# Optimization experiments

Hardware: AMD Instinct MI355X
Metric: run time of the kernel (lower is better)

The kernel has to match this reference:

```python
import jax, jax.numpy as jnp
import numpy as np

B, T, O = 32, 2048, 18            # batch, triples per graph, hardcoded object count
DIN1, H, DOUT = 1500, 512, 512    # net1 input dim is hardcoded 1500 in the source

def _kaiming(key, fan_in, fan_out):
    return jax.random.normal(key, (fan_in, fan_out), jnp.float32) * np.sqrt(2.0 / fan_in)

def setup_inputs() -> dict:
    key = jax.random.key(0)
    ks = jax.random.split(key, 8)
    trip = jax.random.normal(ks[0], (B, T, DIN1), jnp.float32)
    index = jax.random.randint(ks[1], (B, T, 2), 0, O)
    rel_lens = jax.random.randint(ks[2], (B,), 0, T)
    # net1: 1500 -> H -> 2H+Dout (ReLU after every layer incl. last)
    w1a = _kaiming(ks[3], DIN1, H); b1a = jnp.zeros((H,), jnp.float32)
    w1b = _kaiming(ks[4], H, 2 * H + DOUT); b1b = jnp.zeros((2 * H + DOUT,), jnp.float32)
    # net2: H -> H -> Dout (ReLU after every layer incl. last)
    w2a = _kaiming(ks[5], H, H); b2a = jnp.zeros((H,), jnp.float32)
    w2b = _kaiming(ks[6], H, DOUT); b2b = jnp.zeros((DOUT,), jnp.float32)
    return dict(trip=trip, index=index, rel_lens=rel_lens,
                w1a=w1a, b1a=b1a, w1b=w1b, b1b=b1b,
                w2a=w2a, b2a=b2a, w2b=w2b, b2b=b2b)

def reference(trip, index, rel_lens, w1a, b1a, w1b, b1b, w2a, b2a, w2b, b2b):
    # net1 MLP over all triples: [B,T,1500] -> [B,T,2H+Dout]
    h = jax.nn.relu(trip @ w1a + b1a)
    new_t = jax.nn.relu(h @ w1b + b1b)
    s_vecs = new_t[..., :H]              # [B,T,H] subject
    p_vecs = new_t[..., H:H + DOUT]      # [B,T,Dout] predicate (returned as-is)
    o_vecs = new_t[..., H + DOUT:]       # [B,T,H] object
    # mask out triples beyond rel_lens[i]
    mask = (jnp.arange(T)[None, :] < rel_lens[:, None]).astype(new_t.dtype)  # [B,T]
    oh_s = jax.nn.one_hot(index[..., 0], O, dtype=new_t.dtype) * mask[..., None]  # [B,T,O]
    oh_o = jax.nn.one_hot(index[..., 1], O, dtype=new_t.dtype) * mask[..., None]
    # per-batch scatter_add pooling into the O=18 object slots
    contrib = (jnp.einsum('bto,bth->boh', oh_s, s_vecs)
               + jnp.einsum('bto,bth->boh', oh_o, o_vecs))  # [B,O,H]
    # original code never resets pooled_obj_vecs inside the batch loop ->
    # accumulation is CUMULATIVE over batch items
    pooled = jnp.cumsum(contrib, axis=0)  # [B,O,H]
    # net2 MLP on each cumulative pool
    h2 = jax.nn.relu(pooled @ w2a + b2a)
    new_obj = jax.nn.relu(h2 @ w2b + b2b)  # [B,O,Dout]
    return new_obj, p_vecs
```

## Files before the change

### kernel.cpp

```cpp
#include <hip/hip_runtime.h>
#include <hip/hip_bf16.h>

#define NBATCH 32
#define NTIME  2048
#define NOBJ   18
#define KIN    1500
#define NH     512
#define NTOT   1536
#define NM     65536

typedef __attribute__((ext_vector_type(4))) float f32x4;
typedef __attribute__((ext_vector_type(8))) short s16x8;
typedef __attribute__((ext_vector_type(4))) short s16x4;

static __device__ __forceinline__ short f2bf(float f) {
  union { float f; unsigned u; } v; v.f = f;
  unsigned r = v.u + 0x7fffu + ((v.u >> 16) & 1u);
  return (short)(r >> 16);
}

static __device__ __forceinline__ void gload_lds16(const short* g, short* l) {
  __builtin_amdgcn_global_load_lds(
      (const __attribute__((address_space(1))) unsigned int*)(g),
      (__attribute__((address_space(3))) unsigned int*)(l), 16, 0, 0);
}

__global__ void k_prep(const float* __restrict__ src, short* __restrict__ dst,
                       int K, int Nsrc, int nkt, int total) {
  int i = blockIdx.x * 256 + threadIdx.x;
  if (i >= total) return;
  int chunk = i >> 14, off = i & 16383;
  int row = off >> 6, kcp = off & 63;
  int kc = kcp ^ ((row & 7) << 3);
  int cb = chunk / nkt, kt = chunk - cb * nkt;
  int n = cb * 256 + row, k = kt * 64 + kc;
  dst[i] = (k < K) ? f2bf(src[(size_t)k * Nsrc + n]) : (short)0;
}

__launch_bounds__(512, 2)
__global__ void k_gemm1(const float* __restrict__ A, const short* __restrict__ Bc,
                        const float* __restrict__ bias, short* __restrict__ Hc) {
  __shared__ short lA[2][64 * 64];
  __shared__ short lB[2][256 * 64];
  const int g = blockIdx.x;
  const int lid = (g & 7) * 256 + (g >> 3);
  const int rb = lid >> 1, cb = lid & 1;
  const int m0 = rb * 64, n0 = cb * 256;
  const int tid = threadIdx.x;
  const int lane = tid & 63, w = tid >> 6;
  const int wr = w >> 2, wc = w & 3;
  const int rlane = lane & 15, ksel = (lane >> 4) * 8;
  const int arow = tid >> 4;
  const int akq  = (tid & 15) * 4;
  const short* bchunk = Bc + (size_t)(cb * 24) * 16384;

  f32x4 acc[2][4] = {};
  float4 av[2];

  auto issue_stage = [&](int nb, int kt) {
    const int kbase = kt * 64;
    const bool fullq = (kt < 23) | (akq <= 24);
#pragma unroll
    for (int ri = 0; ri < 2; ++ri) {
      const float* p = A + (size_t)(m0 + arow + ri * 32) * KIN + kbase + akq;
      av[ri] = fullq ? *(const float4*)p : make_float4(0.f, 0.f, 0.f, 0.f);
    }
    const short* src = bchunk + (size_t)kt * 16384 + tid * 8;
#pragma unroll
    for (int i = 0; i < 4; ++i)
      gload_lds16(src + i * 4096, &lB[nb][tid * 8 + i * 4096]);
  };
  auto write_stage = [&](int nb) {
#pragma unroll
    for (int ri = 0; ri < 2; ++ri) {
      int row = arow + ri * 32;
      s16x4 h4;
      h4[0] = f2bf(av[ri].x); h4[1] = f2bf(av[ri].y);
      h4[2] = f2bf(av[ri].z); h4[3] = f2bf(av[ri].w);
      *(s16x4*)&lA[nb][row * 64 + (akq ^ ((row & 7) << 3))] = h4;
    }
  };
  auto compute = [&](int cu) {
#pragma unroll
    for (int j = 0; j < 2; ++j) {
      int k0 = j * 32 + ksel;
      s16x8 af[2], bfr[4];
#pragma unroll
      for (int m = 0; m < 2; ++m) {
        int row = wr * 32 + m * 16 + rlane;
        af[m] = *(const s16x8*)&lA[cu][row * 64 + (k0 ^ ((row & 7) << 3))];
      }
#pragma unroll
      for (int n = 0; n < 4; ++n) {
        int row = wc * 64 + n * 16 + rlane;
        bfr[n] = *(const s16x8*)&lB[cu][row * 64 + (k0 ^ ((row & 7) << 3))];
      }
#pragma unroll
      for (int m = 0; m < 2; ++m)
#pragma unroll
        for (int n = 0; n < 4; ++n)
          acc[m][n] = __builtin_amdgcn_mfma_f32_16x16x32_bf16(af[m], bfr[n], acc[m][n], 0, 0, 0);
    }
  };

  issue_stage(0, 0);
  write_stage(0);
  asm volatile("s_waitcnt vmcnt(0)" ::: "memory");
  __syncthreads();
  for (int kt = 0; kt < 24; ++kt) {
    const int cu = kt & 1;
    if (kt < 23) issue_stage(cu ^ 1, kt + 1);
    compute(cu);
    if (kt < 23) {
      write_stage(cu ^ 1);
      asm volatile("s_waitcnt vmcnt(0)" ::: "memory");
      __syncthreads();
    }
  }

#pragma unroll
  for (int n = 0; n < 4; ++n) {
    int c = n0 + wc * 64 + n * 16 + rlane;
    float bv = bias[c];
#pragma unroll
    for (int m = 0; m < 2; ++m) {
      int rbase = m0 + wr * 32 + m * 16 + ((lane >> 4) << 2);
#pragma unroll
      for (int q = 0; q < 4; ++q) {
        int r = rbase + q;
        float v = acc[m][n][q] + bv;
        v = v > 0.f ? v : 0.f;
        Hc[(size_t)(((r >> 7) * 8 + (c >> 6)) * 8192) + (r & 127) * 64 +
           ((c & 63) ^ ((r & 7) << 3))] = f2bf(v);
      }
    }
  }
}

__launch_bounds__(512, 2)
__global__ void k_gemm2(const short* __restrict__ Ac, const short* __restrict__ Bc,
                        const float* __restrict__ bias, const int* __restrict__ index,
                        const int* __restrict__ rel_lens,
                        float* __restrict__ contrib, float* __restrict__ out) {
  __shared__ short lA[2][64 * 64];
  __shared__ short lB[2][256 * 64];
  const int g = blockIdx.x;
  const int lid = (g & 7) * 768 + (g >> 3);
  const int rb = lid / 6, cb = lid - rb * 6;
  const int m0 = rb * 64, n0 = cb * 256;
  const int tid = threadIdx.x;
  const int lane = tid & 63, w = tid >> 6;
  const int wr = w >> 2, wc = w & 3;
  const int rlane = lane & 15, ksel = (lane >> 4) * 8;
  const short* achunk = Ac + (size_t)((m0 >> 7) * 8) * 8192 + (m0 & 127) * 64;
  const short* bchunk = Bc + (size_t)(cb * 8) * 16384;

  f32x4 acc[2][4] = {};

  auto issue_stage = [&](int nb, int kt) {
    gload_lds16(achunk + (size_t)kt * 8192 + tid * 8, &lA[nb][tid * 8]);
    const short* src = bchunk + (size_t)kt * 16384 + tid * 8;
#pragma unroll
    for (int i = 0; i < 4; ++i)
      gload_lds16(src + i * 4096, &lB[nb][tid * 8 + i * 4096]);
  };
  auto compute = [&](int cu) {
#pragma unroll
    for (int j = 0; j < 2; ++j) {
      int k0 = j * 32 + ksel;
      s16x8 af[2], bfr[4];
#pragma unroll
      for (int m = 0; m < 2; ++m) {
        int row = wr * 32 + m * 16 + rlane;
        af[m] = *(const s16x8*)&lA[cu][row * 64 + (k0 ^ ((row & 7) << 3))];
      }
#pragma unroll
      for (int n = 0; n < 4; ++n) {
        int row = wc * 64 + n * 16 + rlane;
        bfr[n] = *(const s16x8*)&lB[cu][row * 64 + (k0 ^ ((row & 7) << 3))];
      }
#pragma unroll
      for (int m = 0; m < 2; ++m)
#pragma unroll
        for (int n = 0; n < 4; ++n)
          acc[m][n] = __builtin_amdgcn_mfma_f32_16x16x32_bf16(af[m], bfr[n], acc[m][n], 0, 0, 0);
    }
  };

  issue_stage(0, 0);
  asm volatile("s_waitcnt vmcnt(0)" ::: "memory");
  __syncthreads();
  for (int kt = 0; kt < 8; ++kt) {
    const int cu = kt & 1;
    if (kt < 7) issue_stage(cu ^ 1, kt + 1);
    compute(cu);
    if (kt < 7) {
      asm volatile("s_waitcnt vmcnt(0)" ::: "memory");
      __syncthreads();
    }
  }

  const int region = n0 >> 9;
  float bv[4]; int cg[4];
#pragma unroll
  for (int n = 0; n < 4; ++n) { cg[n] = n0 + wc * 64 + n * 16 + rlane; bv[n] = bias[cg[n]]; }

  if (region == 1) {
    float* po = out + (size_t)NBATCH * NOBJ * NH;
#pragma unroll
    for (int m = 0; m < 2; ++m) {
      int rbase = m0 + wr * 32 + m * 16 + ((lane >> 4) << 2);
#pragma unroll
      for (int q = 0; q < 4; ++q) {
#pragma unroll
        for (int n = 0; n < 4; ++n) {
          float v = acc[m][n][q] + bv[n];
          v = v > 0.f ? v : 0.f;
          po[(size_t)(rbase + q) * NH + (cg[n] & 511)] = v;
        }
      }
    }
  } else {
    const int sel = region >> 1;
    const int b = m0 >> 11;
    const int rel = rel_lens[b];
#pragma unroll
    for (int m = 0; m < 2; ++m) {
      int rbase = m0 + wr * 32 + m * 16 + ((lane >> 4) << 2);
#pragma unroll
      for (int q = 0; q < 4; ++q) {
        int r = rbase + q;
        if ((r & 2047) < rel) {
          int idx = index[2 * r + sel];
          float* dst = contrib + ((b * NOBJ + idx) << 9);
#pragma unroll
          for (int n = 0; n < 4; ++n) {
            float v = acc[m][n][q] + bv[n];
            v = v > 0.f ? v : 0.f;
            atomicAdd(dst + (cg[n] & 511), v);
          }
        }
      }
    }
  }
}

__global__ void k_cumsum(const float* __restrict__ contrib, float* __restrict__ pooled) {
  int i = blockIdx.x * 256 + threadIdx.x;
  if (i >= NOBJ * NH) return;
  float a = 0.f;
#pragma unroll
  for (int b = 0; b < NBATCH; ++b) {
    a += contrib[b * (NOBJ * NH) + i];
    pooled[b * (NOBJ * NH) + i] = a;
  }
}

__global__ void k_mlp2(const float* __restrict__ pooled,
                       const float* __restrict__ w2a, const float* __restrict__ b2a,
                       const float* __restrict__ w2b, const float* __restrict__ b2b,
                       float* __restrict__ out) {
  __shared__ float pr[NH];
  __shared__ float hr[NH];
  int row = blockIdx.x;
  int tid = threadIdx.x;
  pr[tid]       = pooled[(size_t)row * NH + tid];
  pr[tid + 256] = pooled[(size_t)row * NH + tid + 256];
  __syncthreads();
  float s0 = 0.f, s1 = 0.f;
  for (int k = 0; k < NH; ++k) {
    float p = pr[k];
    s0 += p * w2a[k * NH + tid];
    s1 += p * w2a[k * NH + tid + 256];
  }
  s0 += b2a[tid]; s1 += b2a[tid + 256];
  hr[tid]       = s0 > 0.f ? s0 : 0.f;
  hr[tid + 256] = s1 > 0.f ? s1 : 0.f;
  __syncthreads();
  s0 = 0.f; s1 = 0.f;
  for (int k = 0; k < NH; ++k) {
    float h = hr[k];
    s0 += h * w2b[k * NH + tid];
    s1 += h * w2b[k * NH + tid + 256];
  }
  s0 += b2b[tid]; s1 += b2b[tid + 256];
  out[(size_t)row * NH + tid]       = s0 > 0.f ? s0 : 0.f;
  out[(size_t)row * NH + tid + 256] = s1 > 0.f ? s1 : 0.f;
}

extern "C" void kernel_launch(void* const* d_in, const int* in_sizes, int n_in,
                              void* d_out, int out_size, void* d_ws, size_t ws_size,
                              hipStream_t stream) {
  const float* trip     = (const float*)d_in[0];
  const int*   index    = (const int*)d_in[1];
  const int*   rel_lens = (const int*)d_in[2];
  const float* w1a      = (const float*)d_in[3];
  const float* b1a      = (const float*)d_in[4];
  const float* w1b      = (const float*)d_in[5];
  const float* b1b      = (const float*)d_in[6];
  const float* w2a      = (const float*)d_in[7];
  const float* b2a      = (const float*)d_in[8];
  const float* w2b      = (const float*)d_in[9];
  const float* b2b      = (const float*)d_in[10];
  float* out = (float*)d_out;

  char* ws = (char*)d_ws;
  short* wt1a    = (short*)(ws);
  short* wt1b    = (short*)(ws + 1572864);
  short* hbuf    = (short*)(ws + 3145728);
  float* contrib = (float*)(ws + 70254592);
  float* pooled  = contrib + NBATCH * NOBJ * NH;

  k_prep<<<3072, 256, 0, stream>>>(w1a, wt1a, KIN, NH, 24, NH * 1536);
  k_prep<<<3072, 256, 0, stream>>>(w1b, wt1b, NH, NTOT, 8, NTOT * NH);
  hipMemsetAsync(contrib, 0, (size_t)NBATCH * NOBJ * NH * sizeof(float), stream);
  k_gemm1<<<2048, 512, 0, stream>>>(trip, wt1a, b1a, hbuf);
  k_gemm2<<<6144, 512, 0, stream>>>(hbuf, wt1b, b1b, index, rel_lens, contrib, out);
  k_cumsum<<<36, 256, 0, stream>>>(contrib, pooled);
  k_mlp2<<<576, 256, 0, stream>>>(pooled, w2a, b2a, w2b, b2b, out);
}
```

Before: 480.4 us.

## Enlarge GEMM tiles to 256x256 with quadrant-interleaved loads and MFMA

Both GEMM kernels move from 64x256 to 256x256 output tiles, giving each wave 8x4 accumulators so every LDS fragment feeds more MFMAs. The K-loop is split into four quadrant phases that interleave half-tile global-to-LDS loads with MFMA work, using partial vmcnt waits, raw barriers and s_setprio around the MFMA bursts. The layout of the intermediate H buffer changes to 256-row chunks to match. The goal is higher arithmetic intensity and less global and LDS traffic per FLOP. The cost is fewer blocks (512 and 1536), much higher register pressure, larger LDS use and fragile hand-tuned wait counts.

```diff
diff --git a/kernel.cpp b/kernel.cpp
--- a/kernel.cpp
+++ b/kernel.cpp
@@ -40,97 +40,133 @@
 __launch_bounds__(512, 2)
 __global__ void k_gemm1(const float* __restrict__ A, const short* __restrict__ Bc,
                         const float* __restrict__ bias, short* __restrict__ Hc) {
-  __shared__ short lA[2][64 * 64];
+  __shared__ short lA[2][256 * 64];
   __shared__ short lB[2][256 * 64];
   const int g = blockIdx.x;
-  const int lid = (g & 7) * 256 + (g >> 3);
+  const int lid = (g & 7) * 64 + (g >> 3);
   const int rb = lid >> 1, cb = lid & 1;
-  const int m0 = rb * 64, n0 = cb * 256;
+  const int m0 = rb * 256, n0 = cb * 256;
   const int tid = threadIdx.x;
   const int lane = tid & 63, w = tid >> 6;
   const int wr = w >> 2, wc = w & 3;
   const int rlane = lane & 15, ksel = (lane >> 4) * 8;
+  const int swz = (rlane & 7) << 3;
+  const int kx0 = ksel ^ swz, kx1 = (32 | ksel) ^ swz;
   const int arow = tid >> 4;
   const int akq  = (tid & 15) * 4;
   const short* bchunk = Bc + (size_t)(cb * 24) * 16384;
 
-  f32x4 acc[2][4] = {};
-  float4 av[2];
-
-  auto issue_stage = [&](int nb, int kt) {
+  f32x4 acc[8][4] = {};
+  float4 av[8];
+  s16x8 af[4][2];
+  s16x8 bfr[2][2];
+
+  auto issueA = [&](int kt) {
     const int kbase = kt * 64;
     const bool fullq = (kt < 23) | (akq <= 24);
 #pragma unroll
-    for (int ri = 0; ri < 2; ++ri) {
-      const float* p = A + (size_t)(m0 + arow + ri * 32) * KIN + kbase + akq;
-      av[ri] = fullq ? *(const float4*)p : make_float4(0.f, 0.f, 0.f, 0.f);
-    }
-    const short* src = bchunk + (size_t)kt * 16384 + tid * 8;
-#pragma unroll
-    for (int i = 0; i < 4; ++i)
-      gload_lds16(src + i * 4096, &lB[nb][tid * 8 + i * 4096]);
-  };
-  auto write_stage = [&](int nb) {
-#pragma unroll
-    for (int ri = 0; ri < 2; ++ri) {
-      int row = arow + ri * 32;
+    for (int i = 0; i < 8; ++i) {
+      const float* p = A + (size_t)(m0 + arow + i * 32) * KIN + kbase + akq;
+      av[i] = fullq ? *(const float4*)p : make_float4(0.f, 0.f, 0.f, 0.f);
+    }
+  };
+  auto writeA = [&](int nb) {
+#pragma unroll
+    for (int i = 0; i < 8; ++i) {
+      int r = arow + i * 32;
       s16x4 h4;
-      h4[0] = f2bf(av[ri].x); h4[1] = f2bf(av[ri].y);
-      h4[2] = f2bf(av[ri].z); h4[3] = f2bf(av[ri].w);
-      *(s16x4*)&lA[nb][row * 64 + (akq ^ ((row & 7) << 3))] = h4;
-    }
-  };
-  auto compute = [&](int cu) {
-#pragma unroll
-    for (int j = 0; j < 2; ++j) {
-      int k0 = j * 32 + ksel;
-      s16x8 af[2], bfr[4];
-#pragma unroll
-      for (int m = 0; m < 2; ++m) {
-        int row = wr * 32 + m * 16 + rlane;
-        af[m] = *(const s16x8*)&lA[cu][row * 64 + (k0 ^ ((row & 7) << 3))];
-      }
-#pragma unroll
-      for (int n = 0; n < 4; ++n) {
-        int row = wc * 64 + n * 16 + rlane;
-        bfr[n] = *(const s16x8*)&lB[cu][row * 64 + (k0 ^ ((row & 7) << 3))];
-      }
-#pragma unroll
-      for (int m = 0; m < 2; ++m)
-#pragma unroll
-        for (int n = 0; n < 4; ++n)
-          acc[m][n] = __builtin_amdgcn_mfma_f32_16x16x32_bf16(af[m], bfr[n], acc[m][n], 0, 0, 0);
-    }
-  };
-
-  issue_stage(0, 0);
-  write_stage(0);
-  asm volatile("s_waitcnt vmcnt(0)" ::: "memory");
-  __syncthreads();
-  for (int kt = 0; kt < 24; ++kt) {
-    const int cu = kt & 1;
-    if (kt < 23) issue_stage(cu ^ 1, kt + 1);
-    compute(cu);
-    if (kt < 23) {
-      write_stage(cu ^ 1);
-      asm volatile("s_waitcnt vmcnt(0)" ::: "memory");
-      __syncthreads();
-    }
-  }
+      h4[0] = f2bf(av[i].x); h4[1] = f2bf(av[i].y);
+      h4[2] = f2bf(av[i].z); h4[3] = f2bf(av[i].w);
+      *(s16x4*)&lA[nb][r * 64 + (akq ^ ((r & 7) << 3))] = h4;
+    }
+  };
+  auto issueB = [&](int nb, int kt, int h) {
+    const short* src = bchunk + (size_t)kt * 16384 + h * 8192 + tid * 8;
+#pragma unroll
+    for (int j = 0; j < 2; ++j)
+      gload_lds16(src + j * 4096, &lB[nb][h * 8192 + tid * 8 + j * 4096]);
+  };
+  auto readA = [&](int cu, int rh) {
+#pragma unroll
+    for (int mm = 0; mm < 4; ++mm) {
+      int ro = (rh * 128 + wr * 64 + mm * 16 + rlane) * 64;
+      af[mm][0] = *(const s16x8*)&lA[cu][ro + kx0];
+      af[mm][1] = *(const s16x8*)&lA[cu][ro + kx1];
+    }
+  };
+  auto readB = [&](int cu, int ch) {
+#pragma unroll
+    for (int qn = 0; qn < 2; ++qn) {
+      int ro = (ch * 128 + wc * 32 + qn * 16 + rlane) * 64;
+      bfr[qn][0] = *(const s16x8*)&lB[cu][ro + kx0];
+      bfr[qn][1] = *(const s16x8*)&lB[cu][ro + kx1];
+    }
+  };
+  auto mfma_quad = [&](int rh, int ch) {
+    __builtin_amdgcn_s_setprio(1);
+#pragma unroll
+    for (int j = 0; j < 2; ++j)
+#pragma unroll
+      for (int mm = 0; mm < 4; ++mm)
+#pragma unroll
+        for (int qn = 0; qn < 2; ++qn)
+          acc[rh * 4 + mm][ch * 2 + qn] = __builtin_amdgcn_mfma_f32_16x16x32_bf16(
+              af[mm][j], bfr[qn][j], acc[rh * 4 + mm][ch * 2 + qn], 0, 0, 0);
+    __builtin_amdgcn_s_setprio(0);
+  };
+
+  issueA(0);
+  issueB(0, 0, 0);
+  issueB(0, 0, 1);
+  writeA(0);
+  asm volatile("s_waitcnt lgkmcnt(0)" ::: "memory");
+
+#define G1_TILE(KT, W0S, W1S, HASNEXT)                                  \
+  {                                                                     \
+    const int cu = (KT) & 1, nb = cu ^ 1;                               \
+    asm volatile("s_waitcnt vmcnt(" W0S ")" ::: "memory");              \
+    __builtin_amdgcn_s_barrier();                                       \
+    asm volatile("" ::: "memory");                                      \
+    if (HASNEXT) issueA((KT) + 1);                                      \
+    readA(cu, 0); readB(cu, 0);                                         \
+    mfma_quad(0, 0);                                                    \
+    asm volatile("s_waitcnt vmcnt(" W1S ")" ::: "memory");              \
+    __builtin_amdgcn_s_barrier();                                       \
+    asm volatile("" ::: "memory");                                      \
+    if (HASNEXT) issueB(nb, (KT) + 1, 0);                               \
+    readB(cu, 1);                                                       \
+    mfma_quad(0, 1);                                                    \
+    __builtin_amdgcn_s_barrier();                                       \
+    asm volatile("" ::: "memory");                                      \
+    if (HASNEXT) issueB(nb, (KT) + 1, 1);                               \
+    readA(cu, 1);                                                       \
+    mfma_quad(1, 1);                                                    \
+    __builtin_amdgcn_s_barrier();                                       \
+    asm volatile("" ::: "memory");                                      \
+    if (HASNEXT) writeA(nb);                                            \
+    readB(cu, 0);                                                       \
+    mfma_quad(1, 0);                                                    \
+    if (HASNEXT) asm volatile("s_waitcnt lgkmcnt(0)" ::: "memory");     \
+  }
+
+#pragma unroll 1
+  for (int kt = 0; kt < 23; ++kt) G1_TILE(kt, "2", "8", 1);
+  G1_TILE(23, "2", "0", 0);
+#undef G1_TILE
 
 #pragma unroll
   for (int n = 0; n < 4; ++n) {
-    int c = n0 + wc * 64 + n * 16 + rlane;
+    int c = n0 + (n >> 1) * 128 + wc * 32 + (n & 1) * 16 + rlane;
     float bv = bias[c];
 #pragma unroll
-    for (int m = 0; m < 2; ++m) {
-      int rbase = m0 + wr * 32 + m * 16 + ((lane >> 4) << 2);
+    for (int m = 0; m < 8; ++m) {
+      int rbase = m0 + (m >> 2) * 128 + wr * 64 + (m & 3) * 16 + ((lane >> 4) << 2);
 #pragma unroll
       for (int q = 0; q < 4; ++q) {
         int r = rbase + q;
         float v = acc[m][n][q] + bv;
         v = v > 0.f ? v : 0.f;
-        Hc[(size_t)(((r >> 7) * 8 + (c >> 6)) * 8192) + (r & 127) * 64 +
+        Hc[(size_t)(((r >> 8) * 8 + (c >> 6)) * 16384) + (r & 255) * 64 +
            ((c & 63) ^ ((r & 7) << 3))] = f2bf(v);
       }
     }
@@ -142,74 +178,115 @@
                         const float* __restrict__ bias, const int* __restrict__ index,
                         const int* __restrict__ rel_lens,
                         float* __restrict__ contrib, float* __restrict__ out) {
-  __shared__ short lA[2][64 * 64];
+  __shared__ short lA[2][256 * 64];
   __shared__ short lB[2][256 * 64];
   const int g = blockIdx.x;
-  const int lid = (g & 7) * 768 + (g >> 3);
+  const int lid = (g & 7) * 192 + (g >> 3);
   const int rb = lid / 6, cb = lid - rb * 6;
-  const int m0 = rb * 64, n0 = cb * 256;
+  const int m0 = rb * 256;
   const int tid = threadIdx.x;
   const int lane = tid & 63, w = tid >> 6;
   const int wr = w >> 2, wc = w & 3;
   const int rlane = lane & 15, ksel = (lane >> 4) * 8;
-  const short* achunk = Ac + (size_t)((m0 >> 7) * 8) * 8192 + (m0 & 127) * 64;
+  const int swz = (rlane & 7) << 3;
+  const int kx0 = ksel ^ swz, kx1 = (32 | ksel) ^ swz;
+  const short* achunk = Ac + (size_t)(rb * 8) * 16384;
   const short* bchunk = Bc + (size_t)(cb * 8) * 16384;
 
-  f32x4 acc[2][4] = {};
-
-  auto issue_stage = [&](int nb, int kt) {
-    gload_lds16(achunk + (size_t)kt * 8192 + tid * 8, &lA[nb][tid * 8]);
-    const short* src = bchunk + (size_t)kt * 16384 + tid * 8;
-#pragma unroll
-    for (int i = 0; i < 4; ++i)
-      gload_lds16(src + i * 4096, &lB[nb][tid * 8 + i * 4096]);
-  };
-  auto compute = [&](int cu) {
-#pragma unroll
-    for (int j = 0; j < 2; ++j) {
-      int k0 = j * 32 + ksel;
-      s16x8 af[2], bfr[4];
-#pragma unroll
-      for (int m = 0; m < 2; ++m) {
-        int row = wr * 32 + m * 16 + rlane;
-        af[m] = *(const s16x8*)&lA[cu][row * 64 + (k0 ^ ((row & 7) << 3))];
-      }
-#pragma unroll
-      for (int n = 0; n < 4; ++n) {
-        int row = wc * 64 + n * 16 + rlane;
-        bfr[n] = *(const s16x8*)&lB[cu][row * 64 + (k0 ^ ((row & 7) << 3))];
-      }
-#pragma unroll
-      for (int m = 0; m < 2; ++m)
-#pragma unroll
-        for (int n = 0; n < 4; ++n)
-          acc[m][n] = __builtin_amdgcn_mfma_f32_16x16x32_bf16(af[m], bfr[n], acc[m][n], 0, 0, 0);
-    }
-  };
-
-  issue_stage(0, 0);
-  asm volatile("s_waitcnt vmcnt(0)" ::: "memory");
-  __syncthreads();
-  for (int kt = 0; kt < 8; ++kt) {
-    const int cu = kt & 1;
-    if (kt < 7) issue_stage(cu ^ 1, kt + 1);
-    compute(cu);
-    if (kt < 7) {
-      asm volatile("s_waitcnt vmcnt(0)" ::: "memory");
-      __syncthreads();
-    }
-  }
-
-  const int region = n0 >> 9;
+  f32x4 acc[8][4] = {};
+  s16x8 af[4][2], bf0[2][2], bf1[2][2];
+
+  auto issueA = [&](int nb, int kt, int h) {
+    const short* src = achunk + (size_t)kt * 16384 + h * 8192 + tid * 8;
+#pragma unroll
+    for (int j = 0; j < 2; ++j)
+      gload_lds16(src + j * 4096, &lA[nb][h * 8192 + tid * 8 + j * 4096]);
+  };
+  auto issueB = [&](int nb, int kt, int h) {
+    const short* src = bchunk + (size_t)kt * 16384 + h * 8192 + tid * 8;
+#pragma unroll
+    for (int j = 0; j < 2; ++j)
+      gload_lds16(src + j * 4096, &lB[nb][h * 8192 + tid * 8 + j * 4096]);
+  };
+  auto readA = [&](int cu, int rh) {
+#pragma unroll
+    for (int mm = 0; mm < 4; ++mm) {
+      int ro = (rh * 128 + wr * 64 + mm * 16 + rlane) * 64;
+      af[mm][0] = *(const s16x8*)&lA[cu][ro + kx0];
+      af[mm][1] = *(const s16x8*)&lA[cu][ro + kx1];
+    }
+  };
+  auto readB = [&](int cu, int ch, s16x8 (&dst)[2][2]) {
+#pragma unroll
+    for (int qn = 0; qn < 2; ++qn) {
+      int ro = (ch * 128 + wc * 32 + qn * 16 + rlane) * 64;
+      dst[qn][0] = *(const s16x8*)&lB[cu][ro + kx0];
+      dst[qn][1] = *(const s16x8*)&lB[cu][ro + kx1];
+    }
+  };
+  auto mfma_quad = [&](int rh, int ch, s16x8 (&bfr)[2][2]) {
+    __builtin_amdgcn_s_setprio(1);
+#pragma unroll
+    for (int j = 0; j < 2; ++j)
+#pragma unroll
+      for (int mm = 0; mm < 4; ++mm)
+#pragma unroll
+        for (int qn = 0; qn < 2; ++qn)
+          acc[rh * 4 + mm][ch * 2 + qn] = __builtin_amdgcn_mfma_f32_16x16x32_bf16(
+              af[mm][j], bfr[qn][j], acc[rh * 4 + mm][ch * 2 + qn], 0, 0, 0);
+    __builtin_amdgcn_s_setprio(0);
+  };
+
+  issueA(0, 0, 0);
+  issueB(0, 0, 0);
+  issueB(0, 0, 1);
+  issueA(0, 0, 1);
+
+#define G2_TILE(KT, W0S, W1S, W2S, HASNEXT)                             \
+  {                                                                     \
+    const int cu = (KT) & 1, nb = cu ^ 1;                               \
+    asm volatile("s_waitcnt vmcnt(" W0S ")" ::: "memory");              \
+    __builtin_amdgcn_s_barrier();                                       \
+    asm volatile("" ::: "memory");                                      \
+    if (HASNEXT) issueA(nb, (KT) + 1, 0);                               \
+    readA(cu, 0); readB(cu, 0, bf0);                                    \
+    mfma_quad(0, 0, bf0);                                               \
+    asm volatile("s_waitcnt vmcnt(" W1S ")" ::: "memory");              \
+    __builtin_amdgcn_s_barrier();                                       \
+    asm volatile("" ::: "memory");                                      \
+    if (HASNEXT) issueB(nb, (KT) + 1, 0);                               \
+    readB(cu, 1, bf1);                                                  \
+    mfma_quad(0, 1, bf1);                                               \
+    asm volatile("s_waitcnt vmcnt(" W2S ")" ::: "memory");              \
+    __builtin_amdgcn_s_barrier();                                       \
+    asm volatile("" ::: "memory");                                      \
+    if (HASNEXT) issueB(nb, (KT) + 1, 1);                               \
+    readA(cu, 1);                                                       \
+    mfma_quad(1, 1, bf1);                                               \
+    __builtin_amdgcn_s_barrier();                                       \
+    asm volatile("" ::: "memory");                                      \
+    if (HASNEXT) issueA(nb, (KT) + 1, 1);                               \
+    mfma_quad(1, 0, bf0);                                               \
+  }
+
+#pragma unroll 1
+  for (int kt = 0; kt < 7; ++kt) G2_TILE(kt, "4", "4", "4", 1);
+  G2_TILE(7, "4", "2", "0", 0);
+#undef G2_TILE
+
+  const int region = cb >> 1;
   float bv[4]; int cg[4];
 #pragma unroll
-  for (int n = 0; n < 4; ++n) { cg[n] = n0 + wc * 64 + n * 16 + rlane; bv[n] = bias[cg[n]]; }
+  for (int n = 0; n < 4; ++n) {
+    cg[n] = cb * 256 + (n >> 1) * 128 + wc * 32 + (n & 1) * 16 + rlane;
+    bv[n] = bias[cg[n]];
+  }
 
   if (region == 1) {
     float* po = out + (size_t)NBATCH * NOBJ * NH;
 #pragma unroll
-    for (int m = 0; m < 2; ++m) {
-      int rbase = m0 + wr * 32 + m * 16 + ((lane >> 4) << 2);
+    for (int m = 0; m < 8; ++m) {
+      int rbase = m0 + (m >> 2) * 128 + wr * 64 + (m & 3) * 16 + ((lane >> 4) << 2);
 #pragma unroll
       for (int q = 0; q < 4; ++q) {
 #pragma unroll
@@ -225,8 +302,8 @@
     const int b = m0 >> 11;
     const int rel = rel_lens[b];
 #pragma unroll
-    for (int m = 0; m < 2; ++m) {
-      int rbase = m0 + wr * 32 + m * 16 + ((lane >> 4) << 2);
+    for (int m = 0; m < 8; ++m) {
+      int rbase = m0 + (m >> 2) * 128 + wr * 64 + (m & 3) * 16 + ((lane >> 4) << 2);
 #pragma unroll
       for (int q = 0; q < 4; ++q) {
         int r = rbase + q;
@@ -314,8 +391,8 @@
   k_prep<<<3072, 256, 0, stream>>>(w1a, wt1a, KIN, NH, 24, NH * 1536);
   k_prep<<<3072, 256, 0, stream>>>(w1b, wt1b, NH, NTOT, 8, NTOT * NH);
   hipMemsetAsync(contrib, 0, (size_t)NBATCH * NOBJ * NH * sizeof(float), stream);
-  k_gemm1<<<2048, 512, 0, stream>>>(trip, wt1a, b1a, hbuf);
-  k_gemm2<<<6144, 512, 0, stream>>>(hbuf, wt1b, b1b, index, rel_lens, contrib, out);
+  k_gemm1<<<512, 512, 0, stream>>>(trip, wt1a, b1a, hbuf);
+  k_gemm2<<<1536, 512, 0, stream>>>(hbuf, wt1b, b1b, index, rel_lens, contrib, out);
   k_cumsum<<<36, 256, 0, stream>>>(contrib, pooled);
   k_mlp2<<<576, 256, 0, stream>>>(pooled, w2a, b2a, w2b, b2b, out);
 }
```

Measured after the change: 471.8 us. Within noise of the previous version (-1.8%).
